# Kernel tuning notes

Hardware: AMD Instinct MI355X
Metric: run time of the kernel (lower is better)

The kernel has to match this reference:

```python
import jax, jax.numpy as jnp
import numpy as np

D_MODEL = 1024
N_HEADS = 16
D_KEY = D_MODEL // N_HEADS
NEG = -1e9


def setup_inputs() -> dict:
    key = jax.random.key(0)
    ks = jax.random.split(key, 10)
    B, S = 4, 2048
    s = 0.02
    query = jax.random.normal(ks[0], (B, S, D_MODEL), dtype=jnp.float32)
    # causal mask: 1 where attend allowed, 0 where masked (masked_fill(mask==0, -1e9))
    mask = jnp.tril(jnp.ones((S, S), dtype=jnp.int32))[None, None]
    Wq = jax.random.normal(ks[1], (D_MODEL, D_MODEL), dtype=jnp.float32) * s
    bq = jax.random.normal(ks[2], (D_MODEL,), dtype=jnp.float32) * s
    Wk = jax.random.normal(ks[3], (D_MODEL, D_MODEL), dtype=jnp.float32) * s
    bk = jax.random.normal(ks[4], (D_MODEL,), dtype=jnp.float32) * s
    Wv = jax.random.normal(ks[5], (D_MODEL, D_MODEL), dtype=jnp.float32) * s
    bv = jax.random.normal(ks[6], (D_MODEL,), dtype=jnp.float32) * s
    Wo = jax.random.normal(ks[7], (D_MODEL, D_MODEL), dtype=jnp.float32) * s
    bo = jax.random.normal(ks[8], (D_MODEL,), dtype=jnp.float32) * s
    return {"query": query, "mask": mask, "Wq": Wq, "bq": bq, "Wk": Wk,
            "bk": bk, "Wv": Wv, "bv": bv, "Wo": Wo, "bo": bo}


def _split_heads(x):
    B, S, _ = x.shape
    return x.reshape(B, S, N_HEADS, D_KEY).transpose(0, 2, 1, 3)  # [B,H,S,Dk]


def reference(query, mask, Wq, bq, Wk, bk, Wv, bv, Wo, bo):
    B, S, _ = query.shape
    # torch Linear: x @ W^T + b
    q = _split_heads(query @ Wq.T + bq)
    k = _split_heads(query @ Wk.T + bk)  # self-attention: key_value is None
    v = _split_heads(query @ Wv.T + bv)
    scores = jnp.einsum('bhqd,bhkd->bhqk', q, k) / jnp.sqrt(jnp.float32(D_KEY))
    scores = jnp.where(mask == 0, jnp.float32(NEG), scores)
    weights = jax.nn.softmax(scores, axis=-1)  # dropout=0 (eval)
    attn = jnp.einsum('bhqk,bhkd->bhqd', weights, v)
    merged = attn.transpose(0, 2, 1, 3).reshape(B, S, D_MODEL)
    return merged @ Wo.T + bo
```

## Files before the change

### kernel.cpp

```cpp
#include <hip/hip_runtime.h>
#include <hip/hip_bf16.h>

typedef __attribute__((ext_vector_type(8))) short bf16x8;
typedef __attribute__((ext_vector_type(4))) float f32x4;
typedef __attribute__((ext_vector_type(16))) float f32x16;
typedef __attribute__((ext_vector_type(2))) unsigned int u32x2;

__device__ __forceinline__ float fexp2(float x) { return __builtin_amdgcn_exp2f(x); }

__device__ __forceinline__ ushort f2bf(float x) {
    union { float f; unsigned u; } c; c.f = x;
    unsigned r = c.u + 0x7fff + ((c.u >> 16) & 1);
    return (ushort)(r >> 16);
}

__device__ __forceinline__ unsigned cvtpk(float lo, float hi) {
    unsigned r;
    asm("v_cvt_pk_bf16_f32 %0, %1, %2" : "=v"(r) : "v"(lo), "v"(hi));
    return r;
}

__device__ __forceinline__ void gload16(const void* g, void* l) {
    __builtin_amdgcn_global_load_lds((const __attribute__((address_space(1))) void*)g,
                                     (__attribute__((address_space(3))) void*)l, 16, 0, 0);
}

__device__ __forceinline__ void blockbar() {
    asm volatile("" ::: "memory");
    __builtin_amdgcn_s_barrier();
    asm volatile("" ::: "memory");
}

__global__ void cvt_all(const float* __restrict__ X, const float* __restrict__ wa,
                        const float* __restrict__ wb, const float* __restrict__ wc,
                        const float* __restrict__ wd,
                        ushort* __restrict__ oX, ushort* __restrict__ oWcat,
                        ushort* __restrict__ oWo) {
    const int NX4 = 2097152;
    const int NW4 = 262144;
    const int TOT = NX4 + 4 * NW4;
    int i = blockIdx.x * blockDim.x + threadIdx.x;
    int stride = gridDim.x * blockDim.x;
    for (; i < TOT; i += stride) {
        const float* src; ushort4* dst; int local;
        if (i < NX4) { src = X; local = i; dst = (ushort4*)oX; }
        else {
            int j = i - NX4, sel = j >> 18; local = j & (NW4 - 1);
            src = (sel == 0) ? wa : (sel == 1) ? wb : (sel == 2) ? wc : wd;
            dst = (sel < 3) ? (ushort4*)oWcat + sel * NW4 : (ushort4*)oWo;
        }
        float4 v = ((const float4*)src)[local];
        ushort4 o;
        o.x = f2bf(v.x); o.y = f2bf(v.y); o.z = f2bf(v.z); o.w = f2bf(v.w);
        dst[local] = o;
    }
}

template<int MODE>
__global__ __launch_bounds__(512, 2)
void gemm_p2(const ushort* __restrict__ A, const ushort* __restrict__ Bt,
             const float* __restrict__ bias0, const float* __restrict__ bias1,
             const float* __restrict__ bias2,
             ushort* __restrict__ outb, float* __restrict__ outf,
             int M, int N, int K) {
    __shared__ ushort lds[49152];
    const int t = threadIdx.x, lane = t & 63, w = t >> 6;
    const int wm = w >> 1, wn = w & 1;
    const int l15 = lane & 15, lg = lane >> 4;
    const int sw7 = l15 & 7;

    const int nbx = N >> 7;
    const int nwg = nbx * (M >> 8);
    const int bid = blockIdx.y * nbx + blockIdx.x;
    const int swz = (bid & 7) * (nwg >> 3) + (bid >> 3);
    const int m0 = (swz / nbx) * 256, n0 = (swz % nbx) * 128;

    const int srow = lane >> 3;
    const int gcb = (lane & 7) ^ srow;
    const ushort* gsrc[6];
#pragma unroll
    for (int s = 0; s < 4; s++)
        gsrc[s] = A + (size_t)(m0 + s * 64 + w * 8 + srow) * K + gcb * 8;
#pragma unroll
    for (int s = 0; s < 2; s++)
        gsrc[4 + s] = Bt + (size_t)(n0 + s * 64 + w * 8 + srow) * K + gcb * 8;

#define STAGE(ST, KT) { \
    ushort* dst = &lds[(ST) * 24576 + w * 512]; \
    gload16(gsrc[0] + (KT) * 64, dst); \
    gload16(gsrc[1] + (KT) * 64, dst + 4096); \
    gload16(gsrc[2] + (KT) * 64, dst + 8192); \
    gload16(gsrc[3] + (KT) * 64, dst + 12288); \
    gload16(gsrc[4] + (KT) * 64, dst + 16384); \
    gload16(gsrc[5] + (KT) * 64, dst + 20480); }

    f32x4 acc[4][4] = {};
    const int NT = K >> 6;

    STAGE(0, 0); STAGE(1, 1);

    for (int kt = 0; kt < NT; ++kt) {
        if (kt < NT - 1) asm volatile("s_waitcnt vmcnt(6)" ::: "memory");
        else             asm volatile("s_waitcnt vmcnt(0)" ::: "memory");
        blockbar();

        const ushort* stg = &lds[(kt & 1) * 24576];
        bf16x8 a0[4], b0[4], a1[4], b1[4];
#pragma unroll
        for (int mi = 0; mi < 4; mi++) {
            int row = wm * 64 + mi * 16 + l15;
            a0[mi] = *(const bf16x8*)&stg[row * 64 + ((lg ^ sw7) << 3)];
            a1[mi] = *(const bf16x8*)&stg[row * 64 + (((4 + lg) ^ sw7) << 3)];
        }
#pragma unroll
        for (int ni = 0; ni < 4; ni++) {
            int row = wn * 64 + ni * 16 + l15;
            b0[ni] = *(const bf16x8*)&stg[16384 + row * 64 + ((lg ^ sw7) << 3)];
            b1[ni] = *(const bf16x8*)&stg[16384 + row * 64 + (((4 + lg) ^ sw7) << 3)];
        }

        __builtin_amdgcn_s_setprio(1);
#pragma unroll
        for (int mi = 0; mi < 4; mi++)
#pragma unroll
            for (int ni = 0; ni < 4; ni++)
                acc[mi][ni] = __builtin_amdgcn_mfma_f32_16x16x32_bf16(a0[mi], b0[ni], acc[mi][ni], 0, 0, 0);
        __builtin_amdgcn_s_setprio(0);

        asm volatile("s_waitcnt lgkmcnt(0)" ::: "memory");
        blockbar();
        if (kt + 2 < NT) STAGE((kt & 1), kt + 2);

        __builtin_amdgcn_s_setprio(1);
#pragma unroll
        for (int mi = 0; mi < 4; mi++)
#pragma unroll
            for (int ni = 0; ni < 4; ni++)
                acc[mi][ni] = __builtin_amdgcn_mfma_f32_16x16x32_bf16(a1[mi], b1[ni], acc[mi][ni], 0, 0, 0);
        __builtin_amdgcn_s_setprio(0);
    }
#undef STAGE

#pragma unroll
    for (int mi = 0; mi < 4; mi++)
#pragma unroll
        for (int ni = 0; ni < 4; ni++)
#pragma unroll
            for (int r = 0; r < 4; r++) {
                int gm = m0 + wm * 64 + mi * 16 + lg * 4 + r;
                int gn = n0 + wn * 64 + ni * 16 + l15;
                if (MODE == 0) {
                    const float* bp = (gn < 1024) ? bias0 : ((gn < 2048) ? bias1 : bias2);
                    float v = acc[mi][ni][r] + bp[gn & 1023];
                    if (gn < 1024) v *= 0.18033688011f;
                    int proj = gn >> 10, nn = gn & 1023;
                    int h = nn >> 6, d = nn & 63;
                    int b = gm >> 11, s = gm & 2047;
                    outb[(size_t)proj * 8388608 + ((((size_t)b << 4) + h) * 2048 + s) * 64 + d] = f2bf(v);
                } else {
                    outf[(size_t)gm * N + gn] = acc[mi][ni][r] + bias0[gn];
                }
            }
}

__global__ __launch_bounds__(256, 4)
void attn_fwd(const ushort* __restrict__ Qb, const ushort* __restrict__ Kb,
              const ushort* __restrict__ Vb, ushort* __restrict__ Ab) {
    constexpr int S = 2048;
    __shared__ ushort lds[16384];

    const int bid = blockIdx.x;
    const int qt = 15 - (bid >> 6);
    const int bh = bid & 63;
    const int b = bh >> 4, h = bh & 15;
    const ushort* Qp = Qb + (size_t)bh * S * 64;
    const ushort* Kp = Kb + (size_t)bh * S * 64;
    const ushort* Vp = Vb + (size_t)bh * S * 64;

    const int t = threadIdx.x, lane = t & 63, w = t >> 6;
    const int l15 = lane & 15, l31 = lane & 31, hi = lane >> 5, g = lane >> 4;

    int koff[2], voff[2];
#pragma unroll
    for (int i = 0; i < 2; i++) {
        int row = (w * 2 + i) * 8 + (lane >> 3);
        int gg = (lane & 7) ^ ((row ^ (row >> 3)) & 7);
        koff[i] = row * 64 + gg * 8;
    }
#pragma unroll
    for (int it = 0; it < 2; it++) {
        int T = (it * 4 + w) * 64 + lane;
        int kvb = T >> 5, db = (T >> 3) & 3, kvr = (T >> 1) & 3, dh = T & 1;
        voff[it] = (kvb * 4 + kvr) * 64 + db * 16 + dh * 8;
    }
    const unsigned vtbase = (unsigned)(uintptr_t)&lds[8192]
                          + (hi << 10) + ((g & 1) << 7) + (l15 << 3);

    auto stage = [&](int phase, int k0) {
#pragma unroll
        for (int i = 0; i < 2; i++)
            gload16(Kp + (size_t)k0 * 64 + koff[i], &lds[(phase << 12) + ((w * 2 + i) << 9)]);
#pragma unroll
        for (int it = 0; it < 2; it++)
            gload16(Vp + (size_t)k0 * 64 + voff[it], &lds[8192 + (phase << 12) + (((it << 2) + w) << 9)]);
    };

    const int fb = qt * 128 + w * 32;
    const int nt = 2 * qt + 2;

    bf16x8 qf[4];
#pragma unroll
    for (int kc = 0; kc < 4; kc++)
        qf[kc] = *(const bf16x8*)&Qp[(size_t)(fb + l31) * 64 + kc * 16 + hi * 8];

    float m = -3e38f, ls = 0.f;
    f32x16 O0 = {}, O1 = {};

    stage(0, 0);

    for (int tile = 0; tile < nt; tile++) {
        const int phase = tile & 1;
        const int k0 = tile * 64;
        if (tile + 1 < nt) {
            stage(phase ^ 1, (tile + 1) * 64);
            asm volatile("s_waitcnt vmcnt(4)" ::: "memory");
        } else {
            asm volatile("s_waitcnt vmcnt(0)" ::: "memory");
        }
        blockbar();

        if (k0 <= fb + 31) {
            const ushort* Kc = &lds[phase << 12];
            f32x16 s0 = {}, s1 = {};
            {
                bf16x8 kf[4];
#pragma unroll
                for (int kc = 0; kc < 4; kc++) {
                    int row = l31;
                    int sw = (row ^ (row >> 3)) & 7;
                    kf[kc] = *(const bf16x8*)&Kc[row * 64 + (((kc * 2 + hi) ^ sw) << 3)];
                }
                __builtin_amdgcn_s_setprio(1);
#pragma unroll
                for (int kc = 0; kc < 4; kc++)
                    s0 = __builtin_amdgcn_mfma_f32_32x32x16_bf16(kf[kc], qf[kc], s0, 0, 0, 0);
                __builtin_amdgcn_s_setprio(0);
            }
            {
                bf16x8 kf[4];
#pragma unroll
                for (int kc = 0; kc < 4; kc++) {
                    int row = 32 + l31;
                    int sw = (row ^ (row >> 3)) & 7;
                    kf[kc] = *(const bf16x8*)&Kc[row * 64 + (((kc * 2 + hi) ^ sw) << 3)];
                }
                __builtin_amdgcn_s_setprio(1);
#pragma unroll
                for (int kc = 0; kc < 4; kc++)
                    s1 = __builtin_amdgcn_mfma_f32_32x32x16_bf16(kf[kc], qf[kc], s1, 0, 0, 0);
                __builtin_amdgcn_s_setprio(0);
            }

            float pv[32];
            const bool diag = (k0 + 63 > fb);
            const int rel = fb + l31 - k0 - 4 * hi;
#pragma unroll
            for (int r = 0; r < 16; r++) {
                float v0 = s0[r], v1 = s1[r];
                if (diag) {
                    int kvc = (r & 3) + 8 * (r >> 2);
                    if (kvc > rel)      v0 = -1e30f;
                    if (kvc + 32 > rel) v1 = -1e30f;
                }
                pv[r] = v0; pv[16 + r] = v1;
            }
            float mx[16];
#pragma unroll
            for (int i = 0; i < 16; i++) mx[i] = fmaxf(pv[i], pv[i + 16]);
#pragma unroll
            for (int sgap = 8; sgap >= 1; sgap >>= 1)
#pragma unroll
                for (int i = 0; i < sgap; i++) mx[i] = fmaxf(mx[i], mx[i + sgap]);
            float pmax = fmaxf(mx[0], __shfl_xor(mx[0], 32));

            if (!__all(pmax <= m + 8.f)) {
                float mnew = fmaxf(m, pmax);
                float a = fexp2(m - mnew);
                ls *= a;
                float ar[16];
#pragma unroll
                for (int r = 0; r < 16; r++)
                    ar[r] = __shfl(a, (r & 3) + 8 * (r >> 2) + 4 * hi, 32);
#pragma unroll
                for (int r = 0; r < 16; r++) { O0[r] *= ar[r]; O1[r] *= ar[r]; }
                m = mnew;
            }
#pragma unroll
            for (int i = 0; i < 32; i++) pv[i] = fexp2(pv[i] - m);
            float sm[16];
#pragma unroll
            for (int i = 0; i < 16; i++) sm[i] = pv[i] + pv[i + 16];
#pragma unroll
            for (int sgap = 8; sgap >= 1; sgap >>= 1)
#pragma unroll
                for (int i = 0; i < sgap; i++) sm[i] += sm[i + sgap];
            ls += sm[0] + __shfl_xor(sm[0], 32);

            union PAu { bf16x8 v; unsigned wd[4]; } PA[4];
#pragma unroll
            for (int ks = 0; ks < 4; ks++)
#pragma unroll
                for (int i = 0; i < 2; i++) {
                    unsigned xw = cvtpk(pv[8 * ks + 2 * i], pv[8 * ks + 2 * i + 1]);
                    unsigned yw = cvtpk(pv[8 * ks + 2 * i + 4], pv[8 * ks + 2 * i + 5]);
                    asm("v_permlane32_swap_b32 %0, %1" : "+v"(xw), "+v"(yw));
                    PA[ks].wd[i] = xw; PA[ks].wd[2 + i] = yw;
                }

            const unsigned vtb = vtbase + (phase << 13);
            u32x2 vb[16];
#define TRR(idx, OFFSTR) asm volatile("ds_read_b64_tr_b16 %0, %1 offset:" OFFSTR : "=v"(vb[idx]) : "v"(vtb))
            TRR(0, "0");    TRR(1, "512");  TRR(2, "2048"); TRR(3, "2560");
            TRR(4, "4096"); TRR(5, "4608"); TRR(6, "6144"); TRR(7, "6656");
            TRR(8, "256");  TRR(9, "768");  TRR(10, "2304"); TRR(11, "2816");
            TRR(12, "4352"); TRR(13, "4864"); TRR(14, "6400"); TRR(15, "6912");
#undef TRR
            union FragU { bf16x8 v; u32x2 hh[2]; };
            asm volatile("s_waitcnt lgkmcnt(8)" ::: "memory");
            __builtin_amdgcn_sched_barrier(0);
            __builtin_amdgcn_s_setprio(1);
#pragma unroll
            for (int ks = 0; ks < 4; ks++) {
                FragU f; f.hh[0] = vb[ks * 2]; f.hh[1] = vb[ks * 2 + 1];
                O0 = __builtin_amdgcn_mfma_f32_32x32x16_bf16(PA[ks].v, f.v, O0, 0, 0, 0);
            }
            __builtin_amdgcn_s_setprio(0);
            asm volatile("s_waitcnt lgkmcnt(0)" ::: "memory");
            __builtin_amdgcn_sched_barrier(0);
            __builtin_amdgcn_s_setprio(1);
#pragma unroll
            for (int ks = 0; ks < 4; ks++) {
                FragU f; f.hh[0] = vb[8 + ks * 2]; f.hh[1] = vb[8 + ks * 2 + 1];
                O1 = __builtin_amdgcn_mfma_f32_32x32x16_bf16(PA[ks].v, f.v, O1, 0, 0, 0);
            }
            __builtin_amdgcn_s_setprio(0);
        }
        blockbar();
    }

    float inv[16];
#pragma unroll
    for (int r = 0; r < 16; r++)
        inv[r] = __builtin_amdgcn_rcpf(__shfl(ls, (r & 3) + 8 * (r >> 2) + 4 * hi, 32));
#pragma unroll
    for (int r = 0; r < 16; r++) {
        int q = fb + (r & 3) + 8 * (r >> 2) + 4 * hi;
        size_t base = ((size_t)b * 2048 + q) * 1024 + h * 64;
        Ab[base + l31]      = f2bf(O0[r] * inv[r]);
        Ab[base + 32 + l31] = f2bf(O1[r] * inv[r]);
    }
}

extern "C" void kernel_launch(void* const* d_in, const int* in_sizes, int n_in,
                              void* d_out, int out_size, void* d_ws, size_t ws_size,
                              hipStream_t stream) {
    const float* query = (const float*)d_in[0];
    const float* Wq = (const float*)d_in[2];
    const float* bq = (const float*)d_in[3];
    const float* Wk = (const float*)d_in[4];
    const float* bk = (const float*)d_in[5];
    const float* Wv = (const float*)d_in[6];
    const float* bv = (const float*)d_in[7];
    const float* Wo = (const float*)d_in[8];
    const float* bo = (const float*)d_in[9];
    float* out = (float*)d_out;

    char* ws = (char*)d_ws;
    const size_t SZ_X = 8192ull * 1024 * 2;
    const size_t SZ_W = 1024ull * 1024 * 2;
    ushort* Xb   = (ushort*)(ws);
    ushort* Wcat = (ushort*)(ws + SZ_X);
    ushort* Wob  = (ushort*)(ws + SZ_X + 3 * SZ_W);
    ushort* QKVb = (ushort*)(ws + SZ_X + 4 * SZ_W);
    ushort* Ab   = (ushort*)(ws + 4 * SZ_X + 4 * SZ_W);

    cvt_all<<<2048, 256, 0, stream>>>(query, Wq, Wk, Wv, Wo, Xb, Wcat, Wob);

    gemm_p2<0><<<dim3(3072 / 128, 8192 / 256), 512, 0, stream>>>(
        Xb, Wcat, bq, bk, bv, QKVb, nullptr, 8192, 3072, 1024);

    attn_fwd<<<1024, 256, 0, stream>>>(QKVb, QKVb + 8388608, QKVb + 2 * 8388608, Ab);

    gemm_p2<1><<<dim3(1024 / 128, 8192 / 256), 512, 0, stream>>>(
        Ab, Wob, bo, nullptr, nullptr, nullptr, out, 8192, 1024, 1024);
}
```

Measured before the change: 163.1 us.

## Add 256x256-tile eight-phase pipelined GEMM for the QKV projection

Replaces the templated 256x128 GEMM used for the fused QKV projection with a dedicated kernel using 256x256 output tiles, 8 waves in a 2x4 layout, and a double-buffered LDS schedule. Each K-step is split into four MFMA phases, with global-to-LDS loads for the next tiles interleaved between them. The larger tile raises arithmetic intensity and halves the global traffic per output, at the cost of one block per CU (128KB LDS, 128 accumulators per thread) and fewer workgroups (384). The output projection keeps the old kernel, now de-templated.

Result: no change. 165.0 us (+1.2%).

```diff
diff --git a/kernel.cpp b/kernel.cpp
--- a/kernel.cpp
+++ b/kernel.cpp
@@ -56,13 +56,145 @@
     }
 }
 
-template<int MODE>
+__global__ __launch_bounds__(512, 1)
+void gemm_8ph(const ushort* __restrict__ A, const ushort* __restrict__ Bt,
+              const float* __restrict__ bias0, const float* __restrict__ bias1,
+              const float* __restrict__ bias2,
+              ushort* __restrict__ outb, int M, int N, int K) {
+    __shared__ ushort lds[65536];
+    const int t = threadIdx.x, lane = t & 63, w = t >> 6;
+    const int wm = w >> 2, wn = w & 3;
+    const int l15 = lane & 15, lg = lane >> 4;
+    const int sw7 = l15 & 7;
+
+    const int nbx = N >> 8;
+    const int nwg = nbx * (M >> 8);
+    const int bid = blockIdx.y * nbx + blockIdx.x;
+    const int swz = (bid & 7) * (nwg >> 3) + (bid >> 3);
+    const int m0 = (swz / nbx) * 256, n0 = (swz % nbx) * 256;
+
+    const int row0 = t >> 3, cb0 = t & 7, g0 = cb0 ^ (row0 & 7);
+    const int row1 = row0 + 64, g1 = cb0 ^ (row1 & 7);
+    const ushort* sA[2][2]; const ushort* sB[2][2];
+#pragma unroll
+    for (int h = 0; h < 2; h++) {
+        sA[h][0] = A  + (size_t)(m0 + h * 128 + row0) * K + g0 * 8;
+        sA[h][1] = A  + (size_t)(m0 + h * 128 + row1) * K + g1 * 8;
+        sB[h][0] = Bt + (size_t)(n0 + h * 128 + row0) * K + g0 * 8;
+        sB[h][1] = Bt + (size_t)(n0 + h * 128 + row1) * K + g1 * 8;
+    }
+
+#define STG_A(T, h) { int bb_ = ((T) & 1) * 32768 + (h) * 8192 + t * 8; \
+    gload16(sA[h][0] + (size_t)(T) * 64, &lds[bb_]); \
+    gload16(sA[h][1] + (size_t)(T) * 64, &lds[bb_ + 4096]); }
+#define STG_B(T, h) { int bb_ = ((T) & 1) * 32768 + 16384 + (h) * 8192 + t * 8; \
+    gload16(sB[h][0] + (size_t)(T) * 64, &lds[bb_]); \
+    gload16(sB[h][1] + (size_t)(T) * 64, &lds[bb_ + 4096]); }
+#define RD_A(bb, mi, kk) (*(const bf16x8*)&lds[(bb) + (wm * 128 + (mi) * 16 + l15) * 64 + ((((kk) * 4 + lg) ^ sw7) << 3)])
+#define RD_B(bb, ni, kk) (*(const bf16x8*)&lds[(bb) + 16384 + (wn * 64 + (ni) * 16 + l15) * 64 + ((((kk) * 4 + lg) ^ sw7) << 3)])
+
+    f32x4 acc[8][4] = {};
+    bf16x8 bfr[2][4];
+    const int NT = K >> 6;
+
+    STG_B(0, 0); STG_B(0, 1); STG_A(0, 0); STG_A(0, 1);
+    STG_B(1, 0); STG_B(1, 1); STG_A(1, 0);
+
+    for (int kt = 0; kt < NT; ++kt) {
+        const int bb = (kt & 1) * 32768;
+        if (kt < NT - 1) asm volatile("s_waitcnt vmcnt(6)" ::: "memory");
+        else             asm volatile("s_waitcnt vmcnt(0)" ::: "memory");
+        blockbar();
+
+        bf16x8 af[4];
+#pragma unroll
+        for (int mi = 0; mi < 4; mi++) af[mi] = RD_A(bb, mi, 0);
+#pragma unroll
+        for (int ni = 0; ni < 4; ni++) { bfr[0][ni] = RD_B(bb, ni, 0); bfr[1][ni] = RD_B(bb, ni, 1); }
+        if (kt + 1 < NT) STG_A(kt + 1, 1);
+        blockbar();
+        asm volatile("s_waitcnt lgkmcnt(0)" ::: "memory");
+        __builtin_amdgcn_sched_barrier(0);
+        __builtin_amdgcn_s_setprio(1);
+#pragma unroll
+        for (int mi = 0; mi < 4; mi++)
+#pragma unroll
+            for (int ni = 0; ni < 4; ni++)
+                acc[mi][ni] = __builtin_amdgcn_mfma_f32_16x16x32_bf16(af[mi], bfr[0][ni], acc[mi][ni], 0, 0, 0);
+        __builtin_amdgcn_s_setprio(0);
+        blockbar();
+
+#pragma unroll
+        for (int mi = 0; mi < 4; mi++) af[mi] = RD_A(bb, 4 + mi, 0);
+        if (kt + 2 < NT) STG_B(kt + 2, 0);
+        blockbar();
+        asm volatile("s_waitcnt lgkmcnt(0)" ::: "memory");
+        __builtin_amdgcn_sched_barrier(0);
+        __builtin_amdgcn_s_setprio(1);
+#pragma unroll
+        for (int mi = 0; mi < 4; mi++)
+#pragma unroll
+            for (int ni = 0; ni < 4; ni++)
+                acc[4 + mi][ni] = __builtin_amdgcn_mfma_f32_16x16x32_bf16(af[mi], bfr[0][ni], acc[4 + mi][ni], 0, 0, 0);
+        __builtin_amdgcn_s_setprio(0);
+        blockbar();
+
+#pragma unroll
+        for (int mi = 0; mi < 4; mi++) af[mi] = RD_A(bb, mi, 1);
+        if (kt + 2 < NT) STG_B(kt + 2, 1);
+        blockbar();
+        asm volatile("s_waitcnt lgkmcnt(0)" ::: "memory");
+        __builtin_amdgcn_sched_barrier(0);
+        __builtin_amdgcn_s_setprio(1);
+#pragma unroll
+        for (int mi = 0; mi < 4; mi++)
+#pragma unroll
+            for (int ni = 0; ni < 4; ni++)
+                acc[mi][ni] = __builtin_amdgcn_mfma_f32_16x16x32_bf16(af[mi], bfr[1][ni], acc[mi][ni], 0, 0, 0);
+        __builtin_amdgcn_s_setprio(0);
+        blockbar();
+
+#pragma unroll
+        for (int mi = 0; mi < 4; mi++) af[mi] = RD_A(bb, 4 + mi, 1);
+        if (kt + 2 < NT) STG_A(kt + 2, 0);
+        blockbar();
+        asm volatile("s_waitcnt lgkmcnt(0)" ::: "memory");
+        __builtin_amdgcn_sched_barrier(0);
+        __builtin_amdgcn_s_setprio(1);
+#pragma unroll
+        for (int mi = 0; mi < 4; mi++)
+#pragma unroll
+            for (int ni = 0; ni < 4; ni++)
+                acc[4 + mi][ni] = __builtin_amdgcn_mfma_f32_16x16x32_bf16(af[mi], bfr[1][ni], acc[4 + mi][ni], 0, 0, 0);
+        __builtin_amdgcn_s_setprio(0);
+    }
+#undef STG_A
+#undef STG_B
+#undef RD_A
+#undef RD_B
+
+#pragma unroll
+    for (int mi = 0; mi < 8; mi++)
+#pragma unroll
+        for (int ni = 0; ni < 4; ni++)
+#pragma unroll
+            for (int r = 0; r < 4; r++) {
+                int gm = m0 + wm * 128 + mi * 16 + lg * 4 + r;
+                int gn = n0 + wn * 64 + ni * 16 + l15;
+                const float* bp = (gn < 1024) ? bias0 : ((gn < 2048) ? bias1 : bias2);
+                float v = acc[mi][ni][r] + bp[gn & 1023];
+                if (gn < 1024) v *= 0.18033688011f;
+                int proj = gn >> 10, nn = gn & 1023;
+                int h = nn >> 6, d = nn & 63;
+                int b = gm >> 11, s = gm & 2047;
+                outb[(size_t)proj * 8388608 + ((((size_t)b << 4) + h) * 2048 + s) * 64 + d] = f2bf(v);
+            }
+}
+
 __global__ __launch_bounds__(512, 2)
 void gemm_p2(const ushort* __restrict__ A, const ushort* __restrict__ Bt,
-             const float* __restrict__ bias0, const float* __restrict__ bias1,
-             const float* __restrict__ bias2,
-             ushort* __restrict__ outb, float* __restrict__ outf,
-             int M, int N, int K) {
+             const float* __restrict__ bias0,
+             float* __restrict__ outf, int M, int N, int K) {
     __shared__ ushort lds[49152];
     const int t = threadIdx.x, lane = t & 63, w = t >> 6;
     const int wm = w >> 1, wn = w & 1;
@@ -149,17 +281,7 @@
             for (int r = 0; r < 4; r++) {
                 int gm = m0 + wm * 64 + mi * 16 + lg * 4 + r;
                 int gn = n0 + wn * 64 + ni * 16 + l15;
-                if (MODE == 0) {
-                    const float* bp = (gn < 1024) ? bias0 : ((gn < 2048) ? bias1 : bias2);
-                    float v = acc[mi][ni][r] + bp[gn & 1023];
-                    if (gn < 1024) v *= 0.18033688011f;
-                    int proj = gn >> 10, nn = gn & 1023;
-                    int h = nn >> 6, d = nn & 63;
-                    int b = gm >> 11, s = gm & 2047;
-                    outb[(size_t)proj * 8388608 + ((((size_t)b << 4) + h) * 2048 + s) * 64 + d] = f2bf(v);
-                } else {
-                    outf[(size_t)gm * N + gn] = acc[mi][ni][r] + bias0[gn];
-                }
+                outf[(size_t)gm * N + gn] = acc[mi][ni][r] + bias0[gn];
             }
 }
 
@@ -386,11 +508,11 @@
 
     cvt_all<<<2048, 256, 0, stream>>>(query, Wq, Wk, Wv, Wo, Xb, Wcat, Wob);
 
-    gemm_p2<0><<<dim3(3072 / 128, 8192 / 256), 512, 0, stream>>>(
-        Xb, Wcat, bq, bk, bv, QKVb, nullptr, 8192, 3072, 1024);
+    gemm_8ph<<<dim3(3072 / 256, 8192 / 256), 512, 0, stream>>>(
+        Xb, Wcat, bq, bk, bv, QKVb, 8192, 3072, 1024);
 
     attn_fwd<<<1024, 256, 0, stream>>>(QKVb, QKVb + 8388608, QKVb + 2 * 8388608, Ab);
 
-    gemm_p2<1><<<dim3(1024 / 128, 8192 / 256), 512, 0, stream>>>(
-        Ab, Wob, bo, nullptr, nullptr, nullptr, out, 8192, 1024, 1024);
-}
+    gemm_p2<<<dim3(1024 / 128, 8192 / 256), 512, 0, stream>>>(
+        Ab, Wob, bo, out, 8192, 1024, 1024);
+}
```
